# Kernel optimization log

Measured on AMD Instinct MI355X. Metric: run time of the kernel, lower is better.

The kernel has to match this reference:

```python
import jax, jax.numpy as jnp
import numpy as np

DMODEL = 1024
H = 16
DK = DMODEL // H


def setup_inputs() -> dict:
    key = jax.random.key(0)
    ks = jax.random.split(key, 11)
    B, S = 4, 2048
    scale = 1.0 / np.sqrt(DMODEL)
    inp = {
        'Q': jax.random.normal(ks[0], (B, S, DMODEL), jnp.float32),
        'K': jax.random.normal(ks[1], (B, S, DMODEL), jnp.float32),
        'V': jax.random.normal(ks[2], (B, S, DMODEL), jnp.float32),
        'wq_w': jax.random.normal(ks[3], (DMODEL, DMODEL), jnp.float32) * scale,
        'wq_b': jnp.zeros((DMODEL,), jnp.float32),
        'wk_w': jax.random.normal(ks[4], (DMODEL, DMODEL), jnp.float32) * scale,
        'wk_b': jnp.zeros((DMODEL,), jnp.float32),
        'wv_w': jax.random.normal(ks[5], (DMODEL, DMODEL), jnp.float32) * scale,
        'wv_b': jnp.zeros((DMODEL,), jnp.float32),
        'out_w': jax.random.normal(ks[6], (DMODEL, DMODEL), jnp.float32) * scale,
        'out_b': jnp.zeros((DMODEL,), jnp.float32),
    }
    return inp


def _split_heads(x, B):
    # [B, S, dmodel] -> [B, H, S, DK]
    return x.reshape(B, -1, H, DK).transpose(0, 2, 1, 3)


def reference(Q, K, V, wq_w, wq_b, wk_w, wk_b, wv_w, wv_b, out_w, out_b):
    B, S, _ = Q.shape
    q = _split_heads(Q @ wq_w.T + wq_b, B)  # [B,H,S,DK]
    k = _split_heads(K @ wk_w.T + wk_b, B)
    v = _split_heads(V @ wv_w.T + wv_b, B)
    energy = jnp.einsum('bhqd,bhkd->bhqk', q, k) / jnp.sqrt(jnp.asarray(DK, q.dtype))
    attn = jax.nn.softmax(energy, axis=-1)
    context = jnp.einsum('bhqk,bhkd->bhqd', attn, v)  # [B,H,S,DK]
    context = context.transpose(0, 2, 1, 3).reshape(B, S, DMODEL)
    return context @ out_w.T + out_b
```

## Files before the change

### kernel.cpp

```cpp
#include <hip/hip_runtime.h>
#include <hip/hip_bf16.h>
#include <stdint.h>

#define DMODEL 1024
#define SEQ    2048
#define BATCH  4
#define NH     16
#define DKH    64
#define MROWS  (BATCH*SEQ)

typedef unsigned short u16;
typedef __bf16 bf8 __attribute__((ext_vector_type(8)));
typedef float  f4  __attribute__((ext_vector_type(4)));
typedef float  fv4 __attribute__((ext_vector_type(4)));
typedef unsigned int u32x4 __attribute__((ext_vector_type(4)));
typedef unsigned int u32x2 __attribute__((ext_vector_type(2)));

__device__ __forceinline__ u16 f2b(float f) {
  __bf16 h = (__bf16)f;
  return __builtin_bit_cast(u16, h);
}

__device__ __forceinline__ float exp2_fast(float x) {
#if __has_builtin(__builtin_amdgcn_exp2f)
  return __builtin_amdgcn_exp2f(x);
#else
  return exp2f(x);
#endif
}

__device__ __forceinline__ void plswap32(unsigned& a, unsigned& b) {
#if __has_builtin(__builtin_amdgcn_permlane32_swap)
  u32x2 r = __builtin_amdgcn_permlane32_swap(a, b, false, false);
  a = r[0]; b = r[1];
#else
  asm("v_permlane32_swap_b32 %0, %1" : "+v"(a), "+v"(b));
#endif
}
__device__ __forceinline__ void plswap16(unsigned& a, unsigned& b) {
#if __has_builtin(__builtin_amdgcn_permlane16_swap)
  u32x2 r = __builtin_amdgcn_permlane16_swap(a, b, false, false);
  a = r[0]; b = r[1];
#else
  asm("v_permlane16_swap_b32 %0, %1" : "+v"(a), "+v"(b));
#endif
}

#define GLL16(gp, lp) __builtin_amdgcn_global_load_lds( \
    (const __attribute__((address_space(1))) void*)(gp), \
    (__attribute__((address_space(3))) void*)(lp), 16, 0, 0)

#define MFMA16(a, b, c) __builtin_amdgcn_mfma_f32_16x16x32_bf16((a), (b), (c), 0, 0, 0)

struct CvtArgs {
  const float* src[7];
  u16* dst[7];
  int n8[7];
};

__global__ __launch_bounds__(256) void cvt_all(CvtArgs a) {
  const int r = blockIdx.y;
  const float* __restrict__ s = a.src[r];
  u16* __restrict__ d = a.dst[r];
  const int n8 = a.n8[r];
  for (int i = blockIdx.x * 256 + threadIdx.x; i < n8; i += gridDim.x * 256) {
    fv4 x = *(const fv4*)(s + (size_t)i * 8);
    fv4 y = *(const fv4*)(s + (size_t)i * 8 + 4);
    u32x4 o;
    o[0] = (unsigned)f2b(x[0]) | ((unsigned)f2b(x[1]) << 16);
    o[1] = (unsigned)f2b(x[2]) | ((unsigned)f2b(x[3]) << 16);
    o[2] = (unsigned)f2b(y[0]) | ((unsigned)f2b(y[1]) << 16);
    o[3] = (unsigned)f2b(y[2]) | ((unsigned)f2b(y[3]) << 16);
    *(u32x4*)(d + (size_t)i * 8) = o;
  }
}

template<int MODE>
__device__ __forceinline__ void gemm_core(const u16* __restrict__ A,
                                          const u16* __restrict__ Bw,
                                          const float* __restrict__ bias,
                                          void* __restrict__ Cout,
                                          int bx, int by) {
  __shared__ u16 As[128 * 32];
  __shared__ u16 Bs[128 * 32];
  const int tid = threadIdx.x;
  const int w = tid >> 6, l = tid & 63, g = l >> 4, ln = l & 15;
  const int m0 = by * 128, n0 = bx * 128;
  const int wm = (w >> 1) * 64, wn = (w & 1) * 64;
  const f4 zero = {0.f, 0.f, 0.f, 0.f};
  f4 acc[4][4];
#pragma unroll
  for (int i = 0; i < 4; ++i)
#pragma unroll
    for (int j = 0; j < 4; ++j) acc[i][j] = zero;

  for (int ks = 0; ks < DMODEL / 32; ++ks) {
    __syncthreads();
#pragma unroll
    for (int p = 0; p < 2; ++p) {
      int j = p * 256 + tid;
      int row = j >> 2, cs = j & 3;
      int sc = cs ^ ((row >> 1) & 3);
      GLL16(A + (size_t)(m0 + row) * DMODEL + ks * 32 + sc * 8,
            &As[(p * 256 + w * 64) * 8]);
      GLL16(Bw + (size_t)(n0 + row) * DMODEL + ks * 32 + sc * 8,
            &Bs[(p * 256 + w * 64) * 8]);
    }
    __syncthreads();

    bf8 af[4], bfr[4];
#pragma unroll
    for (int mt = 0; mt < 4; ++mt) {
      int row = wm + mt * 16 + ln;
      af[mt] = *(const bf8*)((const char*)As + row * 64 + ((g ^ ((row >> 1) & 3)) << 4));
    }
#pragma unroll
    for (int nt = 0; nt < 4; ++nt) {
      int row = wn + nt * 16 + ln;
      bfr[nt] = *(const bf8*)((const char*)Bs + row * 64 + ((g ^ ((row >> 1) & 3)) << 4));
    }
#pragma unroll
    for (int mt = 0; mt < 4; ++mt)
#pragma unroll
      for (int nt = 0; nt < 4; ++nt)
        acc[mt][nt] = MFMA16(af[mt], bfr[nt], acc[mt][nt]);
  }

#pragma unroll
  for (int nt = 0; nt < 4; ++nt) {
    int col = n0 + wn + nt * 16 + ln;
    float bv = bias[col];
#pragma unroll
    for (int mt = 0; mt < 4; ++mt) {
      int mrow = m0 + wm + mt * 16 + g * 4;
#pragma unroll
      for (int r = 0; r < 4; ++r) {
        float v = acc[mt][nt][r] + bv;
        int m = mrow + r;
        if (MODE == 2) {
          ((float*)Cout)[(size_t)m * DMODEL + col] = v;
        } else if (MODE == 0) {
          ((u16*)Cout)[(size_t)m * DMODEL + col] = f2b(v);
        } else {
          ((u16*)Cout)[(size_t)m * DMODEL + col] = f2b(v * 0.18033688f);
        }
      }
    }
  }
}

__global__ __launch_bounds__(256) void gemm_qk(
    const u16* __restrict__ Qb, const u16* __restrict__ Kb,
    const u16* __restrict__ Wq, const u16* __restrict__ Wk,
    const float* __restrict__ bq, const float* __restrict__ bk,
    u16* __restrict__ Qp, u16* __restrict__ Kp) {
  const int bid = blockIdx.x;
  const int swz = (bid & 7) * 128 + (bid >> 3);
  const int z = swz >> 9, rem = swz & 511;
  const int by = rem >> 3, bx = rem & 7;
  if (z == 0) gemm_core<3>(Qb, Wq, bq, Qp, bx, by);
  else        gemm_core<0>(Kb, Wk, bk, Kp, bx, by);
}

__global__ __launch_bounds__(256) void gemm_out(
    const u16* __restrict__ Ctx, const u16* __restrict__ Wo,
    const float* __restrict__ bo, float* __restrict__ Out) {
  const int bid = blockIdx.x;
  const int swz = (bid & 7) * 64 + (bid >> 3);
  gemm_core<2>(Ctx, Wo, bo, Out, swz & 7, swz >> 3);
}

__global__ __launch_bounds__(256) void gemm_v(
    const u16* __restrict__ A, const u16* __restrict__ Bw,
    const float* __restrict__ bias, u16* __restrict__ Vt) {
  alignas(16) __shared__ u16 sm[128 * 136];
  u16* As = sm;
  u16* Bs = sm + 4096;
  const int bid = blockIdx.x;
  const int swz = (bid & 7) * 64 + (bid >> 3);
  const int by = swz >> 3, bx = swz & 7;
  const int tid = threadIdx.x;
  const int w = tid >> 6, l = tid & 63, g = l >> 4, ln = l & 15;
  const int m0 = by * 128, n0 = bx * 128;
  const int wm = (w >> 1) * 64, wn = (w & 1) * 64;
  const f4 zero = {0.f, 0.f, 0.f, 0.f};
  f4 acc[4][4];
#pragma unroll
  for (int i = 0; i < 4; ++i)
#pragma unroll
    for (int j = 0; j < 4; ++j) acc[i][j] = zero;

  for (int ks = 0; ks < DMODEL / 32; ++ks) {
    __syncthreads();
#pragma unroll
    for (int p = 0; p < 2; ++p) {
      int j = p * 256 + tid;
      int row = j >> 2, cs = j & 3;
      int sc = cs ^ ((row >> 1) & 3);
      GLL16(A + (size_t)(m0 + row) * DMODEL + ks * 32 + sc * 8,
            &As[(p * 256 + w * 64) * 8]);
      GLL16(Bw + (size_t)(n0 + row) * DMODEL + ks * 32 + sc * 8,
            &Bs[(p * 256 + w * 64) * 8]);
    }
    __syncthreads();

    bf8 af[4], bfr[4];
#pragma unroll
    for (int mt = 0; mt < 4; ++mt) {
      int row = wm + mt * 16 + ln;
      af[mt] = *(const bf8*)((const char*)As + row * 64 + ((g ^ ((row >> 1) & 3)) << 4));
    }
#pragma unroll
    for (int nt = 0; nt < 4; ++nt) {
      int row = wn + nt * 16 + ln;
      bfr[nt] = *(const bf8*)((const char*)Bs + row * 64 + ((g ^ ((row >> 1) & 3)) << 4));
    }
#pragma unroll
    for (int mt = 0; mt < 4; ++mt)
#pragma unroll
      for (int nt = 0; nt < 4; ++nt)
        acc[mt][nt] = MFMA16(af[mt], bfr[nt], acc[mt][nt]);
  }

  __syncthreads();

#pragma unroll
  for (int nt = 0; nt < 4; ++nt) {
    int n_loc = wn + nt * 16 + ln;
    float bv = bias[n0 + n_loc];
#pragma unroll
    for (int mt = 0; mt < 4; ++mt) {
      int m_base = wm + mt * 16 + g * 4;
      u32x2 pk;
      pk[0] = (unsigned)f2b(acc[mt][nt][0] + bv) |
              ((unsigned)f2b(acc[mt][nt][1] + bv) << 16);
      pk[1] = (unsigned)f2b(acc[mt][nt][2] + bv) |
              ((unsigned)f2b(acc[mt][nt][3] + bv) << 16);
      *(u32x2*)&sm[n_loc * 136 + m_base] = pk;
    }
  }
  __syncthreads();

  const int b = m0 >> 11;
  const size_t vbase = (size_t)(b * 1024 + n0);
  const int s0 = m0 & 2047;
#pragma unroll
  for (int it = 0; it < 8; ++it) {
    int task = it * 256 + tid;
    int n = task >> 4, e = task & 15;
    u32x4 v = *(const u32x4*)&sm[n * 136 + e * 8];
    *(u32x4*)&Vt[(vbase + n) * SEQ + s0 + e * 8] = v;
  }
}

__global__ __launch_bounds__(256) void attn_kernel(
    const u16* __restrict__ Qp, const u16* __restrict__ Kp,
    const u16* __restrict__ Vpt, u16* __restrict__ Ctx) {
  __shared__ u16 Klds[2][64 * 64];
  __shared__ u16 Vlds[2][64 * 64];
  const int tid = threadIdx.x, w = tid >> 6, l = tid & 63, g = l >> 4, ln = l & 15;
  const int bid = blockIdx.x;
  const int swz = (bid & 7) * 256 + (bid >> 3);
  const int qc = swz & 31, bh = swz >> 5, h = bh & 15;
  const size_t qkrow = (size_t)(bh >> 4) * SEQ;
  const size_t vrow = (size_t)bh * DKH;
  const int q0 = qc * 64 + w * 16;

  bf8 qf[2];
#pragma unroll
  for (int c = 0; c < 2; ++c)
    qf[c] = *(const bf8*)(Qp + (qkrow + q0 + ln) * DMODEL + h * DKH + c * 32 + g * 8);

  union { u16 s[8]; bf8 f; } ones;
#pragma unroll
  for (int i = 0; i < 8; ++i) ones.s[i] = 0x3F80;

  auto stage = [&](int t, int buf) {
#pragma unroll
    for (int p = 0; p < 2; ++p) {
      int j = p * 256 + tid;
      int row = j >> 3, cs = j & 7;
      int sc = cs ^ (row & 7);
      GLL16(Kp + (qkrow + t * 64 + row) * DMODEL + h * DKH + sc * 8,
            &Klds[buf][(p * 256 + w * 64) * 8]);
      GLL16(Vpt + (vrow + row) * SEQ + t * 64 + sc * 8,
            &Vlds[buf][(p * 256 + w * 64) * 8]);
    }
  };

  const f4 zero = {0.f, 0.f, 0.f, 0.f};
  f4 o[4];
#pragma unroll
  for (int dt = 0; dt < 4; ++dt) o[dt] = zero;
  f4 lacc = zero;

  stage(0, 0);
  __syncthreads();

  for (int t = 0; t < SEQ / 64; ++t) {
    const int cur = t & 1;
    if (t < SEQ / 64 - 1) stage(t + 1, cur ^ 1);

    f4 sf[4];
    __builtin_amdgcn_s_setprio(1);
#pragma unroll
    for (int kt = 0; kt < 4; ++kt) {
      f4 s = zero;
#pragma unroll
      for (int c = 0; c < 2; ++c) {
        int row = kt * 16 + ln;
        bf8 kf = *(const bf8*)((const char*)Klds[cur] + row * 128 +
                               ((((c << 2) | g) ^ (row & 7)) << 4));
        s = MFMA16(kf, qf[c], s);
      }
      sf[kt] = s;
    }
    __builtin_amdgcn_s_setprio(0);

    unsigned pp[4][2];
#pragma unroll
    for (int kt = 0; kt < 4; ++kt) {
      float p0 = exp2_fast(sf[kt][0]);
      float p1 = exp2_fast(sf[kt][1]);
      float p2 = exp2_fast(sf[kt][2]);
      float p3 = exp2_fast(sf[kt][3]);
      pp[kt][0] = (unsigned)f2b(p0) | ((unsigned)f2b(p1) << 16);
      pp[kt][1] = (unsigned)f2b(p2) | ((unsigned)f2b(p3) << 16);
    }

    union { u32x4 u; bf8 f; } pa[2];
#pragma unroll
    for (int c = 0; c < 2; ++c)
#pragma unroll
      for (int r2 = 0; r2 < 2; ++r2) {
        unsigned Areg = pp[2 * c][r2], Breg = pp[2 * c + 1][r2];
        plswap32(Areg, Breg);
        plswap16(Areg, Breg);
        pa[c].u[r2] = Areg;
        pa[c].u[2 + r2] = Breg;
      }

#pragma unroll
    for (int c = 0; c < 2; ++c) {
      __builtin_amdgcn_s_setprio(1);
#pragma unroll
      for (int dt = 0; dt < 4; ++dt) {
        int row = dt * 16 + ln;
        bf8 vf = *(const bf8*)((const char*)Vlds[cur] + row * 128 +
                               ((((c << 2) | g) ^ (row & 7)) << 4));
        o[dt] = MFMA16(pa[c].f, vf, o[dt]);
      }
      lacc = MFMA16(pa[c].f, ones.f, lacc);
      __builtin_amdgcn_s_setprio(0);
    }

    __syncthreads();
  }

  float inv[4];
#pragma unroll
  for (int r = 0; r < 4; ++r) inv[r] = 1.0f / lacc[r];
#pragma unroll
  for (int dt = 0; dt < 4; ++dt)
#pragma unroll
    for (int r = 0; r < 4; ++r)
      Ctx[(qkrow + q0 + g * 4 + r) * DMODEL + h * DKH + dt * 16 + ln] =
          f2b(o[dt][r] * inv[r]);
}

extern "C" void kernel_launch(void* const* d_in, const int* in_sizes, int n_in,
                              void* d_out, int out_size, void* d_ws, size_t ws_size,
                              hipStream_t stream) {
  const float* Q    = (const float*)d_in[0];
  const float* K    = (const float*)d_in[1];
  const float* V    = (const float*)d_in[2];
  const float* wq_w = (const float*)d_in[3];
  const float* wq_b = (const float*)d_in[4];
  const float* wk_w = (const float*)d_in[5];
  const float* wk_b = (const float*)d_in[6];
  const float* wv_w = (const float*)d_in[7];
  const float* wv_b = (const float*)d_in[8];
  const float* ow_w = (const float*)d_in[9];
  const float* ow_b = (const float*)d_in[10];

  char* ws = (char*)d_ws;
  const size_t SZ = (size_t)MROWS * DMODEL * 2;
  const size_t WZ = (size_t)DMODEL * DMODEL * 2;
  u16* Qb  = (u16*)(ws);
  u16* Kb  = (u16*)(ws + SZ);
  u16* Vb  = (u16*)(ws + 2 * SZ);
  u16* Wqb = (u16*)(ws + 3 * SZ);
  u16* Wkb = (u16*)(ws + 3 * SZ + WZ);
  u16* Wvb = (u16*)(ws + 3 * SZ + 2 * WZ);
  u16* Wob = (u16*)(ws + 3 * SZ + 3 * WZ);
  u16* Qp  = (u16*)(ws + 3 * SZ + 4 * WZ);
  u16* Kp  = (u16*)(ws + 4 * SZ + 4 * WZ);
  u16* Vpt = (u16*)(ws + 5 * SZ + 4 * WZ);
  u16* Ctx = (u16*)(ws + 6 * SZ + 4 * WZ);

  CvtArgs ca;
  ca.src[0] = Q;    ca.dst[0] = Qb;  ca.n8[0] = MROWS * DMODEL / 8;
  ca.src[1] = K;    ca.dst[1] = Kb;  ca.n8[1] = MROWS * DMODEL / 8;
  ca.src[2] = V;    ca.dst[2] = Vb;  ca.n8[2] = MROWS * DMODEL / 8;
  ca.src[3] = wq_w; ca.dst[3] = Wqb; ca.n8[3] = DMODEL * DMODEL / 8;
  ca.src[4] = wk_w; ca.dst[4] = Wkb; ca.n8[4] = DMODEL * DMODEL / 8;
  ca.src[5] = wv_w; ca.dst[5] = Wvb; ca.n8[5] = DMODEL * DMODEL / 8;
  ca.src[6] = ow_w; ca.dst[6] = Wob; ca.n8[6] = DMODEL * DMODEL / 8;

  dim3 blk(256);
  cvt_all<<<dim3(512, 7), blk, 0, stream>>>(ca);

  gemm_qk<<<1024, blk, 0, stream>>>(Qb, Kb, Wqb, Wkb, wq_b, wk_b, Qp, Kp);
  gemm_v<<<512, blk, 0, stream>>>(Vb, Wvb, wv_b, Vpt);

  attn_kernel<<<2048, blk, 0, stream>>>(Qp, Kp, Vpt, Ctx);

  gemm_out<<<512, blk, 0, stream>>>(Ctx, Wob, ow_b, (float*)d_out);
}
```

Baseline: 371.1 us.

## Merge Q/K/V projection GEMMs into one launch and deepen K tile to 64

Fuses the separate QK and V projection kernels into a single 1536-block gemm_qkv launch, which removes one kernel launch and the tail between them. The shared GEMM mainloop now loads a 64-wide K slice per iteration with an 8-way XOR swizzle, halving the number of barrier pairs per tile. In exchange, LDS use per block doubles, which may reduce occupancy, and there is still no double buffering.

```diff
diff --git a/kernel.cpp b/kernel.cpp
--- a/kernel.cpp
+++ b/kernel.cpp
@@ -75,57 +75,66 @@
   }
 }
 
-template<int MODE>
-__device__ __forceinline__ void gemm_core(const u16* __restrict__ A,
-                                          const u16* __restrict__ Bw,
-                                          const float* __restrict__ bias,
-                                          void* __restrict__ Cout,
-                                          int bx, int by) {
-  __shared__ u16 As[128 * 32];
-  __shared__ u16 Bs[128 * 32];
+__device__ __forceinline__ void gemm_mainloop(const u16* __restrict__ A,
+                                              const u16* __restrict__ Bw,
+                                              int m0, int n0,
+                                              u16* As, u16* Bs,
+                                              f4 acc[4][4]) {
   const int tid = threadIdx.x;
   const int w = tid >> 6, l = tid & 63, g = l >> 4, ln = l & 15;
-  const int m0 = by * 128, n0 = bx * 128;
   const int wm = (w >> 1) * 64, wn = (w & 1) * 64;
   const f4 zero = {0.f, 0.f, 0.f, 0.f};
-  f4 acc[4][4];
 #pragma unroll
   for (int i = 0; i < 4; ++i)
 #pragma unroll
     for (int j = 0; j < 4; ++j) acc[i][j] = zero;
 
-  for (int ks = 0; ks < DMODEL / 32; ++ks) {
+  for (int ks = 0; ks < DMODEL / 64; ++ks) {
     __syncthreads();
 #pragma unroll
-    for (int p = 0; p < 2; ++p) {
+    for (int p = 0; p < 4; ++p) {
       int j = p * 256 + tid;
-      int row = j >> 2, cs = j & 3;
-      int sc = cs ^ ((row >> 1) & 3);
-      GLL16(A + (size_t)(m0 + row) * DMODEL + ks * 32 + sc * 8,
+      int row = j >> 3, cs = j & 7;
+      int sc = cs ^ (row & 7);
+      GLL16(A + (size_t)(m0 + row) * DMODEL + ks * 64 + sc * 8,
             &As[(p * 256 + w * 64) * 8]);
-      GLL16(Bw + (size_t)(n0 + row) * DMODEL + ks * 32 + sc * 8,
+      GLL16(Bw + (size_t)(n0 + row) * DMODEL + ks * 64 + sc * 8,
             &Bs[(p * 256 + w * 64) * 8]);
     }
     __syncthreads();
 
-    bf8 af[4], bfr[4];
-#pragma unroll
-    for (int mt = 0; mt < 4; ++mt) {
-      int row = wm + mt * 16 + ln;
-      af[mt] = *(const bf8*)((const char*)As + row * 64 + ((g ^ ((row >> 1) & 3)) << 4));
-    }
-#pragma unroll
-    for (int nt = 0; nt < 4; ++nt) {
-      int row = wn + nt * 16 + ln;
-      bfr[nt] = *(const bf8*)((const char*)Bs + row * 64 + ((g ^ ((row >> 1) & 3)) << 4));
-    }
-#pragma unroll
-    for (int mt = 0; mt < 4; ++mt)
-#pragma unroll
-      for (int nt = 0; nt < 4; ++nt)
-        acc[mt][nt] = MFMA16(af[mt], bfr[nt], acc[mt][nt]);
-  }
-
+#pragma unroll
+    for (int kk = 0; kk < 2; ++kk) {
+      bf8 af[4], bfr[4];
+#pragma unroll
+      for (int mt = 0; mt < 4; ++mt) {
+        int row = wm + mt * 16 + ln;
+        af[mt] = *(const bf8*)((const char*)As + row * 128 +
+                               ((((kk << 2) | g) ^ (row & 7)) << 4));
+      }
+#pragma unroll
+      for (int nt = 0; nt < 4; ++nt) {
+        int row = wn + nt * 16 + ln;
+        bfr[nt] = *(const bf8*)((const char*)Bs + row * 128 +
+                                ((((kk << 2) | g) ^ (row & 7)) << 4));
+      }
+#pragma unroll
+      for (int mt = 0; mt < 4; ++mt)
+#pragma unroll
+        for (int nt = 0; nt < 4; ++nt)
+          acc[mt][nt] = MFMA16(af[mt], bfr[nt], acc[mt][nt]);
+    }
+  }
+}
+
+template<int MODE>
+__device__ __forceinline__ void gemm_epilogue(f4 acc[4][4],
+                                              const float* __restrict__ bias,
+                                              void* __restrict__ Cout,
+                                              int m0, int n0) {
+  const int tid = threadIdx.x;
+  const int w = tid >> 6, l = tid & 63, g = l >> 4, ln = l & 15;
+  const int wm = (w >> 1) * 64, wn = (w & 1) * 64;
 #pragma unroll
   for (int nt = 0; nt < 4; ++nt) {
     int col = n0 + wn + nt * 16 + ln;
@@ -149,81 +158,14 @@
   }
 }
 
-__global__ __launch_bounds__(256) void gemm_qk(
-    const u16* __restrict__ Qb, const u16* __restrict__ Kb,
-    const u16* __restrict__ Wq, const u16* __restrict__ Wk,
-    const float* __restrict__ bq, const float* __restrict__ bk,
-    u16* __restrict__ Qp, u16* __restrict__ Kp) {
-  const int bid = blockIdx.x;
-  const int swz = (bid & 7) * 128 + (bid >> 3);
-  const int z = swz >> 9, rem = swz & 511;
-  const int by = rem >> 3, bx = rem & 7;
-  if (z == 0) gemm_core<3>(Qb, Wq, bq, Qp, bx, by);
-  else        gemm_core<0>(Kb, Wk, bk, Kp, bx, by);
-}
-
-__global__ __launch_bounds__(256) void gemm_out(
-    const u16* __restrict__ Ctx, const u16* __restrict__ Wo,
-    const float* __restrict__ bo, float* __restrict__ Out) {
-  const int bid = blockIdx.x;
-  const int swz = (bid & 7) * 64 + (bid >> 3);
-  gemm_core<2>(Ctx, Wo, bo, Out, swz & 7, swz >> 3);
-}
-
-__global__ __launch_bounds__(256) void gemm_v(
-    const u16* __restrict__ A, const u16* __restrict__ Bw,
-    const float* __restrict__ bias, u16* __restrict__ Vt) {
-  alignas(16) __shared__ u16 sm[128 * 136];
-  u16* As = sm;
-  u16* Bs = sm + 4096;
-  const int bid = blockIdx.x;
-  const int swz = (bid & 7) * 64 + (bid >> 3);
-  const int by = swz >> 3, bx = swz & 7;
+__device__ __forceinline__ void gemm_v_epilogue(f4 acc[4][4],
+                                                const float* __restrict__ bias,
+                                                u16* __restrict__ Vt,
+                                                int m0, int n0, u16* sm) {
   const int tid = threadIdx.x;
   const int w = tid >> 6, l = tid & 63, g = l >> 4, ln = l & 15;
-  const int m0 = by * 128, n0 = bx * 128;
   const int wm = (w >> 1) * 64, wn = (w & 1) * 64;
-  const f4 zero = {0.f, 0.f, 0.f, 0.f};
-  f4 acc[4][4];
-#pragma unroll
-  for (int i = 0; i < 4; ++i)
-#pragma unroll
-    for (int j = 0; j < 4; ++j) acc[i][j] = zero;
-
-  for (int ks = 0; ks < DMODEL / 32; ++ks) {
-    __syncthreads();
-#pragma unroll
-    for (int p = 0; p < 2; ++p) {
-      int j = p * 256 + tid;
-      int row = j >> 2, cs = j & 3;
-      int sc = cs ^ ((row >> 1) & 3);
-      GLL16(A + (size_t)(m0 + row) * DMODEL + ks * 32 + sc * 8,
-            &As[(p * 256 + w * 64) * 8]);
-      GLL16(Bw + (size_t)(n0 + row) * DMODEL + ks * 32 + sc * 8,
-            &Bs[(p * 256 + w * 64) * 8]);
-    }
-    __syncthreads();
-
-    bf8 af[4], bfr[4];
-#pragma unroll
-    for (int mt = 0; mt < 4; ++mt) {
-      int row = wm + mt * 16 + ln;
-      af[mt] = *(const bf8*)((const char*)As + row * 64 + ((g ^ ((row >> 1) & 3)) << 4));
-    }
-#pragma unroll
-    for (int nt = 0; nt < 4; ++nt) {
-      int row = wn + nt * 16 + ln;
-      bfr[nt] = *(const bf8*)((const char*)Bs + row * 64 + ((g ^ ((row >> 1) & 3)) << 4));
-    }
-#pragma unroll
-    for (int mt = 0; mt < 4; ++mt)
-#pragma unroll
-      for (int nt = 0; nt < 4; ++nt)
-        acc[mt][nt] = MFMA16(af[mt], bfr[nt], acc[mt][nt]);
-  }
-
   __syncthreads();
-
 #pragma unroll
   for (int nt = 0; nt < 4; ++nt) {
     int n_loc = wn + nt * 16 + ln;
@@ -240,7 +182,6 @@
     }
   }
   __syncthreads();
-
   const int b = m0 >> 11;
   const size_t vbase = (size_t)(b * 1024 + n0);
   const int s0 = m0 & 2047;
@@ -251,6 +192,44 @@
     u32x4 v = *(const u32x4*)&sm[n * 136 + e * 8];
     *(u32x4*)&Vt[(vbase + n) * SEQ + s0 + e * 8] = v;
   }
+}
+
+__global__ __launch_bounds__(256) void gemm_qkv(
+    const u16* __restrict__ Qb, const u16* __restrict__ Kb, const u16* __restrict__ Vb,
+    const u16* __restrict__ Wq, const u16* __restrict__ Wk, const u16* __restrict__ Wv,
+    const float* __restrict__ bq, const float* __restrict__ bk, const float* __restrict__ bv,
+    u16* __restrict__ Qp, u16* __restrict__ Kp, u16* __restrict__ Vpt) {
+  alignas(16) __shared__ u16 sm[17408];
+  u16* As = sm;
+  u16* Bs = sm + 8192;
+  const int bid = blockIdx.x;
+  const int swz = (bid & 7) * 192 + (bid >> 3);
+  const int z = swz >> 9, rem = swz & 511;
+  const int by = rem >> 3, bx = rem & 7;
+  const int m0 = by * 128, n0 = bx * 128;
+  f4 acc[4][4];
+  if (z == 0) {
+    gemm_mainloop(Qb, Wq, m0, n0, As, Bs, acc);
+    gemm_epilogue<3>(acc, bq, Qp, m0, n0);
+  } else if (z == 1) {
+    gemm_mainloop(Kb, Wk, m0, n0, As, Bs, acc);
+    gemm_epilogue<0>(acc, bk, Kp, m0, n0);
+  } else {
+    gemm_mainloop(Vb, Wv, m0, n0, As, Bs, acc);
+    gemm_v_epilogue(acc, bv, Vpt, m0, n0, sm);
+  }
+}
+
+__global__ __launch_bounds__(256) void gemm_out(
+    const u16* __restrict__ Ctx, const u16* __restrict__ Wo,
+    const float* __restrict__ bo, float* __restrict__ Out) {
+  alignas(16) __shared__ u16 sm[16384];
+  const int bid = blockIdx.x;
+  const int swz = (bid & 7) * 64 + (bid >> 3);
+  const int m0 = (swz >> 3) * 128, n0 = (swz & 7) * 128;
+  f4 acc[4][4];
+  gemm_mainloop(Ctx, Wo, m0, n0, sm, sm + 8192, acc);
+  gemm_epilogue<2>(acc, bo, Out, m0, n0);
 }
 
 __global__ __launch_bounds__(256) void attn_kernel(
@@ -410,8 +389,8 @@
   dim3 blk(256);
   cvt_all<<<dim3(512, 7), blk, 0, stream>>>(ca);
 
-  gemm_qk<<<1024, blk, 0, stream>>>(Qb, Kb, Wqb, Wkb, wq_b, wk_b, Qp, Kp);
-  gemm_v<<<512, blk, 0, stream>>>(Vb, Wvb, wv_b, Vpt);
+  gemm_qkv<<<1536, blk, 0, stream>>>(Qb, Kb, Vb, Wqb, Wkb, Wvb,
+                                     wq_b, wk_b, wv_b, Qp, Kp, Vpt);
 
   attn_kernel<<<2048, blk, 0, stream>>>(Qp, Kp, Vpt, Ctx);
 
```

Measured after the change: 358.2 us. 3.5% less time.
